# Performance work log

Measured on AMD Instinct MI355X. Metric: run time of the kernel, lower is better.

## Reference

```python
import jax, jax.numpy as jnp
import numpy as np

KEY_DIM = 64
SCALE_PER_SEQ = 1.0 / np.sqrt(KEY_DIM).astype(np.float32)   # attn_scale_factor_per_seq default
SCALE_OVER_SEQS = 1.0 / np.sqrt(KEY_DIM).astype(np.float32) # attn_scale_factor_over_seqs default


def setup_inputs() -> dict:
    key = jax.random.key(0)
    ks = jax.random.split(key, 6)
    b, i, t, j, d = 8, 256, 64, 256, 256
    kd, vd = KEY_DIM, 64
    return {
        "input_seq": jax.random.normal(ks[0], (b, i, d), dtype=jnp.float32),
        "memory_x": jax.random.normal(ks[1], (b, t, j, d), dtype=jnp.float32),
        "memory_y": jax.random.normal(ks[2], (b, t, j, d), dtype=jnp.float32),
        "Wq": jax.random.normal(ks[3], (d, kd), dtype=jnp.float32) * (1.0 / np.sqrt(d)),
        "bq": jnp.zeros((kd,), dtype=jnp.float32),
        "Wk": jax.random.normal(ks[4], (d, kd), dtype=jnp.float32) * (1.0 / np.sqrt(d)),
        "bk": jnp.zeros((kd,), dtype=jnp.float32),
        "Wv": jax.random.normal(ks[5], (d, vd), dtype=jnp.float32) * (1.0 / np.sqrt(d)),
        "bv": jnp.zeros((vd,), dtype=jnp.float32),
    }


def reference(input_seq, memory_x, memory_y, Wq, bq, Wk, bk, Wv, bv):
    # Dense projections
    queries = input_seq @ Wq + bq            # [b, i, kd]
    keys = memory_x @ Wk + bk                # [b, t, j, kd]
    values = memory_y @ Wv + bv              # [b, t, j, vd]

    # Raw scores between every query and every token of every memory sequence
    attn_mat = jnp.einsum('bik,btjk->btij', queries, keys)  # [b, t, i, j]

    # Level 1: within-sequence attention (softmax over tokens j)
    per_seq_attn = jax.nn.softmax(SCALE_PER_SEQ * attn_mat, axis=-1)
    per_seq_retrieved = jnp.einsum('btij,btjk->btik', per_seq_attn, values)  # [b, t, i, vd]

    # Level 2: over-sequences attention (max over j, softmax over t)
    mem_seq_scores = jnp.max(attn_mat, axis=-1)                      # [b, t, i]
    mem_seq_attn = jax.nn.softmax(SCALE_OVER_SEQS * mem_seq_scores, axis=1)

    retrieved_mems = jnp.einsum('bti,btik->bik', mem_seq_attn, per_seq_retrieved)  # [b, i, vd]
    return retrieved_mems
```

## Files before the change

### kernel.cpp

```cpp
#include <hip/hip_runtime.h>
#include <hip/hip_bf16.h>

#define NB 8
#define NT 64
#define NI 256
#define NJ 256
#define ND 256
#define NKD 64
#define NVD 64
#define SCL 0.125f

typedef __attribute__((ext_vector_type(4))) float f32x4;
typedef __attribute__((ext_vector_type(8))) short bf16x8;
typedef __attribute__((ext_vector_type(4))) short bf16x4;
typedef __attribute__((ext_vector_type(4))) unsigned int uint32x4;

#define MFMA16(A, B, C) __builtin_amdgcn_mfma_f32_16x16x32_bf16((A), (B), (C), 0, 0, 0)

#define R2B 32768

__device__ __forceinline__ unsigned short f2bf(float x) {
  return __builtin_bit_cast(unsigned short, __float2bfloat16(x));
}
__device__ __forceinline__ float bf2f(unsigned short h) {
  return __builtin_bit_cast(float, (unsigned)h << 16);
}
__device__ __forceinline__ void split8(const float* __restrict__ x, bf16x8& hi, bf16x8& lo) {
  #pragma unroll
  for (int e = 0; e < 8; ++e) {
    unsigned short h = f2bf(x[e]);
    hi[e] = (short)h;
    lo[e] = (short)f2bf(x[e] - bf2f(h));
  }
}

__global__ __launch_bounds__(64) void k_prep_projq(
    const float* __restrict__ x, const float* __restrict__ Wq,
    const float* __restrict__ bq,
    const float* __restrict__ Wk, const float* __restrict__ Wv,
    unsigned short* __restrict__ Wkth, unsigned short* __restrict__ Wvth,
    unsigned short* __restrict__ Qh) {
  int lane = threadIdx.x;
  if (blockIdx.x < 256) {
    int t = blockIdx.x * 64 + lane;
    int d = t >> 6, kd = t & 63;
    Wkth[kd * 256 + d] = f2bf(Wk[t]);
    Wvth[kd * 256 + d] = f2bf(Wv[t]);
    return;
  }
  int row = blockIdx.x - 256;
  __shared__ __align__(16) float xs[ND];
  const float* xr = x + (size_t)row * ND;
  #pragma unroll
  for (int cc = 0; cc < 4; ++cc) xs[lane + 64 * cc] = xr[lane + 64 * cc];
  __syncthreads();
  float acc = bq[lane];
  #pragma unroll 4
  for (int d = 0; d < ND; ++d) acc = fmaf(xs[d], Wq[d * NKD + lane], acc);
  Qh[(size_t)row * NKD + lane] = f2bf(acc);
}

__device__ __forceinline__ void stage_plane(
    char* dstb, const unsigned short* __restrict__ Wt, int tid) {
  #pragma unroll
  for (int it = 0; it < 4; ++it) {
    int qq = tid + it * 512;
    int r = qq >> 5, pb = qq & 31;
    uint4 v = *(const uint4*)((const char*)Wt + (size_t)qq * 16);
    *(uint4*)(dstb + r * 512 + ((pb ^ (r & 7)) << 4)) = v;
  }
}

__global__ __launch_bounds__(512, 4) void k_fused(
    const float* __restrict__ Xm, const float* __restrict__ Ym,
    const unsigned short* __restrict__ Wkth, const unsigned short* __restrict__ Wvth,
    const float* __restrict__ bk, const float* __restrict__ bv,
    const unsigned short* __restrict__ Qh,
    unsigned short* __restrict__ R,
    float* __restrict__ Sc) {
  __shared__ __align__(16) char smemb[65536];
  int tid = threadIdx.x;
  int bt = blockIdx.x, b = bt >> 6;
  int w = tid >> 6, lane = tid & 63, c = lane & 15, g = lane >> 4;

  const float* xr0 = Xm + (size_t)bt * 65536 + (size_t)(w * 32 + c) * 256 + g * 8;
  const float* xr1 = xr0 + 16 * 256;
  const float* yr0 = Ym + (size_t)bt * 65536 + (size_t)(w * 32 + c) * 256 + g * 8;
  const float* yr1 = yr0 + 16 * 256;

  float4 xa0 = *(const float4*)(xr0),      xa1 = *(const float4*)(xr0 + 4);
  float4 xa2 = *(const float4*)(xr1),      xa3 = *(const float4*)(xr1 + 4);
  float4 xb0 = *(const float4*)(xr0 + 32), xb1 = *(const float4*)(xr0 + 36);
  float4 xb2 = *(const float4*)(xr1 + 32), xb3 = *(const float4*)(xr1 + 36);
  float4 ya0 = *(const float4*)(yr0),      ya1 = *(const float4*)(yr0 + 4);
  float4 ya2 = *(const float4*)(yr1),      ya3 = *(const float4*)(yr1 + 4);
  float4 yb0 = *(const float4*)(yr0 + 32), yb1 = *(const float4*)(yr0 + 36);
  float4 yb2 = *(const float4*)(yr1 + 32), yb3 = *(const float4*)(yr1 + 36);

  stage_plane(smemb, Wkth, tid);
  stage_plane(smemb + R2B, Wvth, tid);
  __syncthreads();

  f32x4 kacc[4][2];
  f32x4 vacc[2][4];
  #pragma unroll
  for (int mf = 0; mf < 4; ++mf) { kacc[mf][0] = (f32x4)0.f; kacc[mf][1] = (f32x4)0.f; }
  #pragma unroll
  for (int mf = 0; mf < 2; ++mf)
    #pragma unroll
    for (int nf = 0; nf < 4; ++nf) vacc[mf][nf] = (f32x4)0.f;

  #pragma unroll
  for (int ks = 0; ks < 8; ++ks) {
    float x0[8], x1[8];
    if (ks & 1) {
      *(float4*)&x0[0] = xb0; *(float4*)&x0[4] = xb1;
      *(float4*)&x1[0] = xb2; *(float4*)&x1[4] = xb3;
      if (ks < 6) {
        xb0 = *(const float4*)(xr0 + (ks + 2) * 32);
        xb1 = *(const float4*)(xr0 + (ks + 2) * 32 + 4);
        xb2 = *(const float4*)(xr1 + (ks + 2) * 32);
        xb3 = *(const float4*)(xr1 + (ks + 2) * 32 + 4);
      }
    } else {
      *(float4*)&x0[0] = xa0; *(float4*)&x0[4] = xa1;
      *(float4*)&x1[0] = xa2; *(float4*)&x1[4] = xa3;
      if (ks < 6) {
        xa0 = *(const float4*)(xr0 + (ks + 2) * 32);
        xa1 = *(const float4*)(xr0 + (ks + 2) * 32 + 4);
        xa2 = *(const float4*)(xr1 + (ks + 2) * 32);
        xa3 = *(const float4*)(xr1 + (ks + 2) * 32 + 4);
      }
    }
    {
      bf16x8 b0h, b0l, b1h, b1l;
      split8(x0, b0h, b0l);
      split8(x1, b1h, b1l);
      #pragma unroll
      for (int mf = 0; mf < 4; ++mf) {
        int r = mf * 16 + c;
        int ba = r * 512 + (((ks * 4 + g) ^ (r & 7)) << 4);
        bf16x8 awh = *(const bf16x8*)(smemb + ba);
        kacc[mf][0] = MFMA16(awh, b0h, kacc[mf][0]);
        kacc[mf][0] = MFMA16(awh, b0l, kacc[mf][0]);
        kacc[mf][1] = MFMA16(awh, b1h, kacc[mf][1]);
        kacc[mf][1] = MFMA16(awh, b1l, kacc[mf][1]);
      }
    }
    float y0[8], y1[8];
    if (ks & 1) {
      *(float4*)&y0[0] = yb0; *(float4*)&y0[4] = yb1;
      *(float4*)&y1[0] = yb2; *(float4*)&y1[4] = yb3;
      if (ks < 6) {
        yb0 = *(const float4*)(yr0 + (ks + 2) * 32);
        yb1 = *(const float4*)(yr0 + (ks + 2) * 32 + 4);
        yb2 = *(const float4*)(yr1 + (ks + 2) * 32);
        yb3 = *(const float4*)(yr1 + (ks + 2) * 32 + 4);
      }
    } else {
      *(float4*)&y0[0] = ya0; *(float4*)&y0[4] = ya1;
      *(float4*)&y1[0] = ya2; *(float4*)&y1[4] = ya3;
      if (ks < 6) {
        ya0 = *(const float4*)(yr0 + (ks + 2) * 32);
        ya1 = *(const float4*)(yr0 + (ks + 2) * 32 + 4);
        ya2 = *(const float4*)(yr1 + (ks + 2) * 32);
        ya3 = *(const float4*)(yr1 + (ks + 2) * 32 + 4);
      }
    }
    {
      bf16x8 a0h, a0l, a1h, a1l;
      split8(y0, a0h, a0l);
      split8(y1, a1h, a1l);
      #pragma unroll
      for (int nf = 0; nf < 4; ++nf) {
        int r = nf * 16 + c;
        int ba = R2B + r * 512 + (((ks * 4 + g) ^ (r & 7)) << 4);
        bf16x8 bwh = *(const bf16x8*)(smemb + ba);
        vacc[0][nf] = MFMA16(a0h, bwh, vacc[0][nf]);
        vacc[0][nf] = MFMA16(a0l, bwh, vacc[0][nf]);
        vacc[1][nf] = MFMA16(a1h, bwh, vacc[1][nf]);
        vacc[1][nf] = MFMA16(a1l, bwh, vacc[1][nf]);
      }
    }
  }
  bf16x8 qbh[2][2];
  #pragma unroll
  for (int ks = 0; ks < 2; ++ks)
    #pragma unroll
    for (int ic = 0; ic < 2; ++ic) {
      size_t qo = ((size_t)b * NI + w * 32 + ic * 16 + c) * NKD + ks * 32 + g * 8;
      qbh[ks][ic] = *(const bf16x8*)(Qh + qo);
    }
  __syncthreads();

  #pragma unroll
  for (int nf = 0; nf < 2; ++nf) {
    int j = w * 32 + nf * 16 + c;
    #pragma unroll
    for (int mf = 0; mf < 4; ++mf) {
      bf16x4 ph;
      #pragma unroll
      for (int r = 0; r < 4; ++r)
        ph[r] = (short)f2bf(kacc[mf][nf][r] + bk[mf * 16 + g * 4 + r]);
      int pb = mf * 2 + (g >> 1);
      int ba = j * 128 + ((pb ^ (j & 7)) << 4) + (g & 1) * 8;
      *(bf16x4*)(smemb + ba) = ph;
    }
  }
  #pragma unroll
  for (int nf = 0; nf < 4; ++nf) {
    int vd = nf * 16 + c;
    float bs = bv[vd];
    #pragma unroll
    for (int mf = 0; mf < 2; ++mf) {
      bf16x4 ph;
      #pragma unroll
      for (int r = 0; r < 4; ++r) ph[r] = (short)f2bf(vacc[mf][nf][r] + bs);
      int pb = w * 4 + mf * 2 + (g >> 1);
      int ba = R2B + vd * 512 + ((pb ^ (vd & 7)) << 4) + (g & 1) * 8;
      *(bf16x4*)(smemb + ba) = ph;
    }
  }
  __syncthreads();

  #pragma unroll
  for (int ic = 0; ic < 2; ++ic) {
    int i = w * 32 + ic * 16 + c;

    f32x4 sa[16];
    #pragma unroll
    for (int jf = 0; jf < 16; ++jf) sa[jf] = (f32x4)0.f;
    #pragma unroll
    for (int jf = 0; jf < 16; ++jf) {
      int j = jf * 16 + c;
      #pragma unroll
      for (int ks = 0; ks < 2; ++ks) {
        int ba = j * 128 + (((ks * 4 + g) ^ (j & 7)) << 4);
        bf16x8 kh = *(const bf16x8*)(smemb + ba);
        sa[jf] = MFMA16(kh, qbh[ks][ic], sa[jf]);
      }
    }

    float mx = sa[0][0];
    #pragma unroll
    for (int jf = 0; jf < 16; ++jf)
      #pragma unroll
      for (int r = 0; r < 4; ++r) mx = fmaxf(mx, sa[jf][r]);
    mx = fmaxf(mx, __shfl_xor(mx, 16));
    mx = fmaxf(mx, __shfl_xor(mx, 32));
    if (g == 0) Sc[(size_t)bt * NI + i] = mx;
    float sum = 0.f;
    #pragma unroll
    for (int jf = 0; jf < 16; ++jf)
      #pragma unroll
      for (int r = 0; r < 4; ++r) {
        float p = __expf((sa[jf][r] - mx) * SCL);
        sa[jf][r] = p;
        sum += p;
      }
    sum += __shfl_xor(sum, 16);
    sum += __shfl_xor(sum, 32);
    float linv = 1.0f / sum;

    unsigned int plo[16], phi[16];
    #pragma unroll
    for (int jf = 0; jf < 16; ++jf) {
      plo[jf] = (unsigned int)f2bf(sa[jf][0]) | ((unsigned int)f2bf(sa[jf][1]) << 16);
      phi[jf] = (unsigned int)f2bf(sa[jf][2]) | ((unsigned int)f2bf(sa[jf][3]) << 16);
    }

    int srcA = c + 32 * (g & 1);
    int srcB = srcA + 16;
    bool hiH = (g >= 2);

    f32x4 racc[4];
    #pragma unroll
    for (int vf = 0; vf < 4; ++vf) racc[vf] = (f32x4)0.f;
    #pragma unroll
    for (int js = 0; js < 8; ++js) {
      int a0 = __shfl((int)plo[2 * js], srcA);
      int a1 = __shfl((int)phi[2 * js], srcA);
      int a2 = __shfl((int)plo[2 * js], srcB);
      int a3 = __shfl((int)phi[2 * js], srcB);
      int b0 = __shfl((int)plo[2 * js + 1], srcA);
      int b1 = __shfl((int)phi[2 * js + 1], srcA);
      int b2 = __shfl((int)plo[2 * js + 1], srcB);
      int b3 = __shfl((int)phi[2 * js + 1], srcB);
      uint32x4 pw;
      pw[0] = (unsigned int)(hiH ? b0 : a0);
      pw[1] = (unsigned int)(hiH ? b1 : a1);
      pw[2] = (unsigned int)(hiH ? b2 : a2);
      pw[3] = (unsigned int)(hiH ? b3 : a3);
      bf16x8 pf = __builtin_bit_cast(bf16x8, pw);
      #pragma unroll
      for (int vf = 0; vf < 4; ++vf) {
        int vd = vf * 16 + c;
        int vba = R2B + vd * 512 + (((js * 4 + g) ^ (vd & 7)) << 4);
        bf16x8 vh = *(const bf16x8*)(smemb + vba);
        racc[vf] = MFMA16(vh, pf, racc[vf]);
      }
    }

    #pragma unroll
    for (int vf = 0; vf < 4; ++vf) {
      bf16x4 rk;
      #pragma unroll
      for (int r = 0; r < 4; ++r) rk[r] = (short)f2bf(racc[vf][r] * linv);
      *(bf16x4*)(R + ((size_t)bt * NI + i) * NKD + vf * 16 + g * 4) = rk;
    }
  }
}

__global__ __launch_bounds__(256) void k_level2(
    const float* __restrict__ Sc,
    const unsigned short* __restrict__ R,
    float* __restrict__ out) {
  int w = threadIdx.x >> 6, lane = threadIdx.x & 63;
  int bi = blockIdx.x * 4 + w;
  int b = bi >> 8, i = bi & 255;
  float sc = Sc[((size_t)b * NT + lane) * NI + i];
  float mx = sc;
  #pragma unroll
  for (int off = 32; off; off >>= 1) mx = fmaxf(mx, __shfl_xor(mx, off));
  float e = __expf((sc - mx) * SCL);
  float sum = e;
  #pragma unroll
  for (int off = 32; off; off >>= 1) sum += __shfl_xor(sum, off);
  float wn = e / sum;
  float acc = 0.f;
  for (int t = 0; t < NT; ++t) {
    float wt = __shfl(wn, t);
    acc = fmaf(wt, bf2f(R[(((size_t)b * NT + t) * NI + i) * NKD + lane]), acc);
  }
  out[((size_t)b * NI + i) * NVD + lane] = acc;
}

extern "C" void kernel_launch(void* const* d_in, const int* in_sizes, int n_in,
                              void* d_out, int out_size, void* d_ws, size_t ws_size,
                              hipStream_t stream) {
  const float* x   = (const float*)d_in[0];
  const float* mxp = (const float*)d_in[1];
  const float* myp = (const float*)d_in[2];
  const float* Wq  = (const float*)d_in[3];
  const float* bq  = (const float*)d_in[4];
  const float* Wk  = (const float*)d_in[5];
  const float* bk  = (const float*)d_in[6];
  const float* Wv  = (const float*)d_in[7];
  const float* bv  = (const float*)d_in[8];
  float* out = (float*)d_out;

  char* p = (char*)d_ws;
  auto alloc = [&](size_t bytes) { char* r = p; p += (bytes + 255) & ~(size_t)255; return r; };
  unsigned short* Qh   = (unsigned short*)alloc(2048 * 64 * 2);
  unsigned short* Rw   = (unsigned short*)alloc((size_t)131072 * 64 * 2);
  float*          Scw  = (float*)alloc((size_t)131072 * 4);
  unsigned short* Wkth = (unsigned short*)alloc(64 * 256 * 2);
  unsigned short* Wvth = (unsigned short*)alloc(64 * 256 * 2);

  hipLaunchKernelGGL(k_prep_projq, dim3(256 + NB * NI), dim3(64), 0, stream,
                     x, Wq, bq, Wk, Wv, Wkth, Wvth, Qh);
  hipLaunchKernelGGL(k_fused, dim3(NB * NT), dim3(512), 0, stream,
                     mxp, myp, Wkth, Wvth, bk, bv, Qh, Rw, Scw);
  hipLaunchKernelGGL(k_level2, dim3(512), dim3(256), 0, stream, Scw, Rw, out);
}
```

Measured before the change: 94.67 us.

## Fold Wk into queries and compute scores directly against raw memory_x

```diff
diff --git a/kernel.cpp b/kernel.cpp
--- a/kernel.cpp
+++ b/kernel.cpp
@@ -13,11 +13,10 @@
 typedef __attribute__((ext_vector_type(4))) float f32x4;
 typedef __attribute__((ext_vector_type(8))) short bf16x8;
 typedef __attribute__((ext_vector_type(4))) short bf16x4;
-typedef __attribute__((ext_vector_type(4))) unsigned int uint32x4;
 
 #define MFMA16(A, B, C) __builtin_amdgcn_mfma_f32_16x16x32_bf16((A), (B), (C), 0, 0, 0)
 
-#define R2B 32768
+#define XB 32768
 
 __device__ __forceinline__ unsigned short f2bf(float x) {
   return __builtin_bit_cast(unsigned short, __float2bfloat16(x));
@@ -34,18 +33,15 @@
   }
 }
 
-__global__ __launch_bounds__(64) void k_prep_projq(
+__global__ __launch_bounds__(64) void k_prepA(
     const float* __restrict__ x, const float* __restrict__ Wq,
-    const float* __restrict__ bq,
-    const float* __restrict__ Wk, const float* __restrict__ Wv,
-    unsigned short* __restrict__ Wkth, unsigned short* __restrict__ Wvth,
-    unsigned short* __restrict__ Qh) {
+    const float* __restrict__ bq, const float* __restrict__ Wv,
+    unsigned short* __restrict__ Wvth, float* __restrict__ Qf) {
   int lane = threadIdx.x;
   if (blockIdx.x < 256) {
     int t = blockIdx.x * 64 + lane;
-    int d = t >> 6, kd = t & 63;
-    Wkth[kd * 256 + d] = f2bf(Wk[t]);
-    Wvth[kd * 256 + d] = f2bf(Wv[t]);
+    int d = t >> 6, vd = t & 63;
+    Wvth[vd * 256 + d] = f2bf(Wv[t]);
     return;
   }
   int row = blockIdx.x - 256;
@@ -57,257 +53,212 @@
   float acc = bq[lane];
   #pragma unroll 4
   for (int d = 0; d < ND; ++d) acc = fmaf(xs[d], Wq[d * NKD + lane], acc);
-  Qh[(size_t)row * NKD + lane] = f2bf(acc);
-}
-
-__device__ __forceinline__ void stage_plane(
-    char* dstb, const unsigned short* __restrict__ Wt, int tid) {
-  #pragma unroll
-  for (int it = 0; it < 4; ++it) {
-    int qq = tid + it * 512;
-    int r = qq >> 5, pb = qq & 31;
-    uint4 v = *(const uint4*)((const char*)Wt + (size_t)qq * 16);
-    *(uint4*)(dstb + r * 512 + ((pb ^ (r & 7)) << 4)) = v;
-  }
-}
-
-__global__ __launch_bounds__(512, 4) void k_fused(
+  Qf[(size_t)row * NKD + lane] = acc;
+}
+
+__global__ __launch_bounds__(256) void k_prepB(
+    const float* __restrict__ Wk, const float* __restrict__ Qf,
+    unsigned short* __restrict__ Qkw) {
+  __shared__ __align__(16) float qs[8 * 64];
+  int tid = threadIdx.x;
+  size_t bi0 = (size_t)blockIdx.x * 8;
+  qs[tid]       = Qf[bi0 * 64 + tid];
+  qs[tid + 256] = Qf[bi0 * 64 + tid + 256];
+  __syncthreads();
+  int d = tid;
+  float acc[8];
+  #pragma unroll
+  for (int r8 = 0; r8 < 8; ++r8) acc[r8] = 0.f;
+  #pragma unroll 4
+  for (int kc = 0; kc < 16; ++kc) {
+    float4 wv = *(const float4*)(Wk + (size_t)d * 64 + kc * 4);
+    #pragma unroll
+    for (int r8 = 0; r8 < 8; ++r8) {
+      const float* q4 = qs + r8 * 64 + kc * 4;
+      acc[r8] += wv.x * q4[0] + wv.y * q4[1] + wv.z * q4[2] + wv.w * q4[3];
+    }
+  }
+  #pragma unroll
+  for (int r8 = 0; r8 < 8; ++r8)
+    Qkw[(bi0 + r8) * 256 + d] = f2bf(acc[r8]);
+}
+
+__global__ __launch_bounds__(1024) void k_fused(
     const float* __restrict__ Xm, const float* __restrict__ Ym,
-    const unsigned short* __restrict__ Wkth, const unsigned short* __restrict__ Wvth,
-    const float* __restrict__ bk, const float* __restrict__ bv,
-    const unsigned short* __restrict__ Qh,
+    const unsigned short* __restrict__ Wvth, const float* __restrict__ bv,
+    const unsigned short* __restrict__ Qkw,
     unsigned short* __restrict__ R,
     float* __restrict__ Sc) {
-  __shared__ __align__(16) char smemb[65536];
+  __shared__ __align__(16) char smemb[163840];
   int tid = threadIdx.x;
   int bt = blockIdx.x, b = bt >> 6;
   int w = tid >> 6, lane = tid & 63, c = lane & 15, g = lane >> 4;
 
-  const float* xr0 = Xm + (size_t)bt * 65536 + (size_t)(w * 32 + c) * 256 + g * 8;
-  const float* xr1 = xr0 + 16 * 256;
-  const float* yr0 = Ym + (size_t)bt * 65536 + (size_t)(w * 32 + c) * 256 + g * 8;
-  const float* yr1 = yr0 + 16 * 256;
-
-  float4 xa0 = *(const float4*)(xr0),      xa1 = *(const float4*)(xr0 + 4);
-  float4 xa2 = *(const float4*)(xr1),      xa3 = *(const float4*)(xr1 + 4);
-  float4 xb0 = *(const float4*)(xr0 + 32), xb1 = *(const float4*)(xr0 + 36);
-  float4 xb2 = *(const float4*)(xr1 + 32), xb3 = *(const float4*)(xr1 + 36);
-  float4 ya0 = *(const float4*)(yr0),      ya1 = *(const float4*)(yr0 + 4);
-  float4 ya2 = *(const float4*)(yr1),      ya3 = *(const float4*)(yr1 + 4);
-  float4 yb0 = *(const float4*)(yr0 + 32), yb1 = *(const float4*)(yr0 + 36);
-  float4 yb2 = *(const float4*)(yr1 + 32), yb3 = *(const float4*)(yr1 + 36);
-
-  stage_plane(smemb, Wkth, tid);
-  stage_plane(smemb + R2B, Wvth, tid);
-  __syncthreads();
-
-  f32x4 kacc[4][2];
-  f32x4 vacc[2][4];
-  #pragma unroll
-  for (int mf = 0; mf < 4; ++mf) { kacc[mf][0] = (f32x4)0.f; kacc[mf][1] = (f32x4)0.f; }
-  #pragma unroll
-  for (int mf = 0; mf < 2; ++mf)
-    #pragma unroll
-    for (int nf = 0; nf < 4; ++nf) vacc[mf][nf] = (f32x4)0.f;
+  const float* xbase = Xm + (size_t)bt * 65536;
+  const float* yr = Ym + (size_t)bt * 65536 + (size_t)(w * 16 + c) * 256 + g * 8;
+
+  float4 ya0 = *(const float4*)(yr),      ya1 = *(const float4*)(yr + 4);
+  float4 yb0 = *(const float4*)(yr + 32), yb1 = *(const float4*)(yr + 36);
+  float4 xf0 = *(const float4*)(xbase + (size_t)(tid >> 5) * 256 + (tid & 31) * 8);
+  float4 xf1 = *(const float4*)(xbase + (size_t)(tid >> 5) * 256 + (tid & 31) * 8 + 4);
+
+  #pragma unroll
+  for (int it = 0; it < 2; ++it) {
+    int qq = tid + it * 1024;
+    int r = qq >> 5, pb = qq & 31;
+    uint4 v = *(const uint4*)((const char*)Wvth + (size_t)qq * 16);
+    *(uint4*)(smemb + r * 512 + ((pb ^ (r & 7)) << 4)) = v;
+  }
+  __syncthreads();
+
+  f32x4 vacc[4];
+  #pragma unroll
+  for (int nf = 0; nf < 4; ++nf) vacc[nf] = (f32x4)0.f;
 
   #pragma unroll
   for (int ks = 0; ks < 8; ++ks) {
-    float x0[8], x1[8];
-    if (ks & 1) {
-      *(float4*)&x0[0] = xb0; *(float4*)&x0[4] = xb1;
-      *(float4*)&x1[0] = xb2; *(float4*)&x1[4] = xb3;
-      if (ks < 6) {
-        xb0 = *(const float4*)(xr0 + (ks + 2) * 32);
-        xb1 = *(const float4*)(xr0 + (ks + 2) * 32 + 4);
-        xb2 = *(const float4*)(xr1 + (ks + 2) * 32);
-        xb3 = *(const float4*)(xr1 + (ks + 2) * 32 + 4);
-      }
-    } else {
-      *(float4*)&x0[0] = xa0; *(float4*)&x0[4] = xa1;
-      *(float4*)&x1[0] = xa2; *(float4*)&x1[4] = xa3;
-      if (ks < 6) {
-        xa0 = *(const float4*)(xr0 + (ks + 2) * 32);
-        xa1 = *(const float4*)(xr0 + (ks + 2) * 32 + 4);
-        xa2 = *(const float4*)(xr1 + (ks + 2) * 32);
-        xa3 = *(const float4*)(xr1 + (ks + 2) * 32 + 4);
-      }
-    }
-    {
-      bf16x8 b0h, b0l, b1h, b1l;
-      split8(x0, b0h, b0l);
-      split8(x1, b1h, b1l);
-      #pragma unroll
-      for (int mf = 0; mf < 4; ++mf) {
-        int r = mf * 16 + c;
-        int ba = r * 512 + (((ks * 4 + g) ^ (r & 7)) << 4);
-        bf16x8 awh = *(const bf16x8*)(smemb + ba);
-        kacc[mf][0] = MFMA16(awh, b0h, kacc[mf][0]);
-        kacc[mf][0] = MFMA16(awh, b0l, kacc[mf][0]);
-        kacc[mf][1] = MFMA16(awh, b1h, kacc[mf][1]);
-        kacc[mf][1] = MFMA16(awh, b1l, kacc[mf][1]);
-      }
-    }
-    float y0[8], y1[8];
+    float4 cx0 = xf0, cx1 = xf1;
+    int cc = ks * 1024 + tid;
+    if (ks < 7) {
+      int cn = cc + 1024;
+      xf0 = *(const float4*)(xbase + (size_t)(cn >> 5) * 256 + (cn & 31) * 8);
+      xf1 = *(const float4*)(xbase + (size_t)(cn >> 5) * 256 + (cn & 31) * 8 + 4);
+    }
+    float y0[8];
     if (ks & 1) {
       *(float4*)&y0[0] = yb0; *(float4*)&y0[4] = yb1;
-      *(float4*)&y1[0] = yb2; *(float4*)&y1[4] = yb3;
       if (ks < 6) {
-        yb0 = *(const float4*)(yr0 + (ks + 2) * 32);
-        yb1 = *(const float4*)(yr0 + (ks + 2) * 32 + 4);
-        yb2 = *(const float4*)(yr1 + (ks + 2) * 32);
-        yb3 = *(const float4*)(yr1 + (ks + 2) * 32 + 4);
+        yb0 = *(const float4*)(yr + (ks + 2) * 32);
+        yb1 = *(const float4*)(yr + (ks + 2) * 32 + 4);
       }
     } else {
       *(float4*)&y0[0] = ya0; *(float4*)&y0[4] = ya1;
-      *(float4*)&y1[0] = ya2; *(float4*)&y1[4] = ya3;
       if (ks < 6) {
-        ya0 = *(const float4*)(yr0 + (ks + 2) * 32);
-        ya1 = *(const float4*)(yr0 + (ks + 2) * 32 + 4);
-        ya2 = *(const float4*)(yr1 + (ks + 2) * 32);
-        ya3 = *(const float4*)(yr1 + (ks + 2) * 32 + 4);
+        ya0 = *(const float4*)(yr + (ks + 2) * 32);
+        ya1 = *(const float4*)(yr + (ks + 2) * 32 + 4);
       }
     }
     {
-      bf16x8 a0h, a0l, a1h, a1l;
+      int r = cc >> 5, q2 = cc & 31;
+      uint4 xw;
+      xw.x = (unsigned int)f2bf(cx0.x) | ((unsigned int)f2bf(cx0.y) << 16);
+      xw.y = (unsigned int)f2bf(cx0.z) | ((unsigned int)f2bf(cx0.w) << 16);
+      xw.z = (unsigned int)f2bf(cx1.x) | ((unsigned int)f2bf(cx1.y) << 16);
+      xw.w = (unsigned int)f2bf(cx1.z) | ((unsigned int)f2bf(cx1.w) << 16);
+      *(uint4*)(smemb + XB + r * 512 + ((q2 ^ (r & 7)) << 4)) = xw;
+    }
+    {
+      bf16x8 a0h, a0l;
       split8(y0, a0h, a0l);
-      split8(y1, a1h, a1l);
       #pragma unroll
       for (int nf = 0; nf < 4; ++nf) {
         int r = nf * 16 + c;
-        int ba = R2B + r * 512 + (((ks * 4 + g) ^ (r & 7)) << 4);
+        int ba = r * 512 + (((ks * 4 + g) ^ (r & 7)) << 4);
         bf16x8 bwh = *(const bf16x8*)(smemb + ba);
-        vacc[0][nf] = MFMA16(a0h, bwh, vacc[0][nf]);
-        vacc[0][nf] = MFMA16(a0l, bwh, vacc[0][nf]);
-        vacc[1][nf] = MFMA16(a1h, bwh, vacc[1][nf]);
-        vacc[1][nf] = MFMA16(a1l, bwh, vacc[1][nf]);
+        vacc[nf] = MFMA16(a0h, bwh, vacc[nf]);
+        vacc[nf] = MFMA16(a0l, bwh, vacc[nf]);
       }
     }
   }
-  bf16x8 qbh[2][2];
-  #pragma unroll
-  for (int ks = 0; ks < 2; ++ks)
-    #pragma unroll
-    for (int ic = 0; ic < 2; ++ic) {
-      size_t qo = ((size_t)b * NI + w * 32 + ic * 16 + c) * NKD + ks * 32 + g * 8;
-      qbh[ks][ic] = *(const bf16x8*)(Qh + qo);
-    }
-  __syncthreads();
-
-  #pragma unroll
-  for (int nf = 0; nf < 2; ++nf) {
-    int j = w * 32 + nf * 16 + c;
-    #pragma unroll
-    for (int mf = 0; mf < 4; ++mf) {
-      bf16x4 ph;
-      #pragma unroll
-      for (int r = 0; r < 4; ++r)
-        ph[r] = (short)f2bf(kacc[mf][nf][r] + bk[mf * 16 + g * 4 + r]);
-      int pb = mf * 2 + (g >> 1);
-      int ba = j * 128 + ((pb ^ (j & 7)) << 4) + (g & 1) * 8;
-      *(bf16x4*)(smemb + ba) = ph;
-    }
-  }
+  bf16x8 qk[8];
+  #pragma unroll
+  for (int ks = 0; ks < 8; ++ks)
+    qk[ks] = *(const bf16x8*)(Qkw + ((size_t)(b * NI + w * 16 + c)) * 256 + ks * 32 + g * 8);
+  __syncthreads();
+
   #pragma unroll
   for (int nf = 0; nf < 4; ++nf) {
     int vd = nf * 16 + c;
     float bs = bv[vd];
-    #pragma unroll
-    for (int mf = 0; mf < 2; ++mf) {
-      bf16x4 ph;
-      #pragma unroll
-      for (int r = 0; r < 4; ++r) ph[r] = (short)f2bf(vacc[mf][nf][r] + bs);
-      int pb = w * 4 + mf * 2 + (g >> 1);
-      int ba = R2B + vd * 512 + ((pb ^ (vd & 7)) << 4) + (g & 1) * 8;
-      *(bf16x4*)(smemb + ba) = ph;
-    }
-  }
-  __syncthreads();
-
-  #pragma unroll
-  for (int ic = 0; ic < 2; ++ic) {
-    int i = w * 32 + ic * 16 + c;
-
-    f32x4 sa[16];
-    #pragma unroll
-    for (int jf = 0; jf < 16; ++jf) sa[jf] = (f32x4)0.f;
+    bf16x4 ph;
+    #pragma unroll
+    for (int r = 0; r < 4; ++r) ph[r] = (short)f2bf(vacc[nf][r] + bs);
+    int pb = w * 2 + (g >> 1);
+    *(bf16x4*)(smemb + vd * 512 + ((pb ^ (vd & 7)) << 4) + (g & 1) * 8) = ph;
+  }
+  __syncthreads();
+
+  int i = w * 16 + c;
+
+  f32x4 sa[16];
+  #pragma unroll
+  for (int jf = 0; jf < 16; ++jf) sa[jf] = (f32x4)0.f;
+  #pragma unroll
+  for (int ks = 0; ks < 8; ++ks) {
     #pragma unroll
     for (int jf = 0; jf < 16; ++jf) {
-      int j = jf * 16 + c;
-      #pragma unroll
-      for (int ks = 0; ks < 2; ++ks) {
-        int ba = j * 128 + (((ks * 4 + g) ^ (j & 7)) << 4);
-        bf16x8 kh = *(const bf16x8*)(smemb + ba);
-        sa[jf] = MFMA16(kh, qbh[ks][ic], sa[jf]);
-      }
-    }
-
-    float mx = sa[0][0];
-    #pragma unroll
-    for (int jf = 0; jf < 16; ++jf)
-      #pragma unroll
-      for (int r = 0; r < 4; ++r) mx = fmaxf(mx, sa[jf][r]);
-    mx = fmaxf(mx, __shfl_xor(mx, 16));
-    mx = fmaxf(mx, __shfl_xor(mx, 32));
-    if (g == 0) Sc[(size_t)bt * NI + i] = mx;
-    float sum = 0.f;
-    #pragma unroll
-    for (int jf = 0; jf < 16; ++jf)
-      #pragma unroll
-      for (int r = 0; r < 4; ++r) {
-        float p = __expf((sa[jf][r] - mx) * SCL);
-        sa[jf][r] = p;
-        sum += p;
-      }
-    sum += __shfl_xor(sum, 16);
-    sum += __shfl_xor(sum, 32);
-    float linv = 1.0f / sum;
-
-    unsigned int plo[16], phi[16];
-    #pragma unroll
-    for (int jf = 0; jf < 16; ++jf) {
-      plo[jf] = (unsigned int)f2bf(sa[jf][0]) | ((unsigned int)f2bf(sa[jf][1]) << 16);
-      phi[jf] = (unsigned int)f2bf(sa[jf][2]) | ((unsigned int)f2bf(sa[jf][3]) << 16);
-    }
-
-    int srcA = c + 32 * (g & 1);
-    int srcB = srcA + 16;
-    bool hiH = (g >= 2);
-
-    f32x4 racc[4];
-    #pragma unroll
-    for (int vf = 0; vf < 4; ++vf) racc[vf] = (f32x4)0.f;
-    #pragma unroll
-    for (int js = 0; js < 8; ++js) {
-      int a0 = __shfl((int)plo[2 * js], srcA);
-      int a1 = __shfl((int)phi[2 * js], srcA);
-      int a2 = __shfl((int)plo[2 * js], srcB);
-      int a3 = __shfl((int)phi[2 * js], srcB);
-      int b0 = __shfl((int)plo[2 * js + 1], srcA);
-      int b1 = __shfl((int)phi[2 * js + 1], srcA);
-      int b2 = __shfl((int)plo[2 * js + 1], srcB);
-      int b3 = __shfl((int)phi[2 * js + 1], srcB);
-      uint32x4 pw;
-      pw[0] = (unsigned int)(hiH ? b0 : a0);
-      pw[1] = (unsigned int)(hiH ? b1 : a1);
-      pw[2] = (unsigned int)(hiH ? b2 : a2);
-      pw[3] = (unsigned int)(hiH ? b3 : a3);
-      bf16x8 pf = __builtin_bit_cast(bf16x8, pw);
-      #pragma unroll
-      for (int vf = 0; vf < 4; ++vf) {
-        int vd = vf * 16 + c;
-        int vba = R2B + vd * 512 + (((js * 4 + g) ^ (vd & 7)) << 4);
-        bf16x8 vh = *(const bf16x8*)(smemb + vba);
-        racc[vf] = MFMA16(vh, pf, racc[vf]);
-      }
-    }
-
+      int r = jf * 16 + c;
+      bf16x8 xa = *(const bf16x8*)(smemb + XB + r * 512 + (((ks * 4 + g) ^ (r & 7)) << 4));
+      sa[jf] = MFMA16(xa, qk[ks], sa[jf]);
+    }
+  }
+
+  float mx = sa[0][0];
+  #pragma unroll
+  for (int jf = 0; jf < 16; ++jf)
+    #pragma unroll
+    for (int r = 0; r < 4; ++r) mx = fmaxf(mx, sa[jf][r]);
+  mx = fmaxf(mx, __shfl_xor(mx, 16));
+  mx = fmaxf(mx, __shfl_xor(mx, 32));
+  if (g == 0) Sc[(size_t)bt * NI + i] = mx;
+  float sum = 0.f;
+  #pragma unroll
+  for (int jf = 0; jf < 16; ++jf)
+    #pragma unroll
+    for (int r = 0; r < 4; ++r) {
+      float p = __expf((sa[jf][r] - mx) * SCL);
+      sa[jf][r] = p;
+      sum += p;
+    }
+  sum += __shfl_xor(sum, 16);
+  sum += __shfl_xor(sum, 32);
+  float linv = 1.0f / sum;
+
+  unsigned int plo[16], phi[16];
+  #pragma unroll
+  for (int jf = 0; jf < 16; ++jf) {
+    plo[jf] = (unsigned int)f2bf(sa[jf][0]) | ((unsigned int)f2bf(sa[jf][1]) << 16);
+    phi[jf] = (unsigned int)f2bf(sa[jf][2]) | ((unsigned int)f2bf(sa[jf][3]) << 16);
+  }
+
+  int srcA = c + 32 * (g & 1);
+  int srcB = srcA + 16;
+  bool hiH = (g >= 2);
+
+  f32x4 racc[4];
+  #pragma unroll
+  for (int vf = 0; vf < 4; ++vf) racc[vf] = (f32x4)0.f;
+  #pragma unroll
+  for (int js = 0; js < 8; ++js) {
+    int a0 = __shfl((int)plo[2 * js], srcA);
+    int a1 = __shfl((int)phi[2 * js], srcA);
+    int a2 = __shfl((int)plo[2 * js], srcB);
+    int a3 = __shfl((int)phi[2 * js], srcB);
+    int b0 = __shfl((int)plo[2 * js + 1], srcA);
+    int b1 = __shfl((int)phi[2 * js + 1], srcA);
+    int b2 = __shfl((int)plo[2 * js + 1], srcB);
+    int b3 = __shfl((int)phi[2 * js + 1], srcB);
+    unsigned int pw0 = (unsigned int)(hiH ? b0 : a0);
+    unsigned int pw1 = (unsigned int)(hiH ? b1 : a1);
+    unsigned int pw2 = (unsigned int)(hiH ? b2 : a2);
+    unsigned int pw3 = (unsigned int)(hiH ? b3 : a3);
+    uint4 pwv = make_uint4(pw0, pw1, pw2, pw3);
+    bf16x8 pf = __builtin_bit_cast(bf16x8, pwv);
     #pragma unroll
     for (int vf = 0; vf < 4; ++vf) {
-      bf16x4 rk;
-      #pragma unroll
-      for (int r = 0; r < 4; ++r) rk[r] = (short)f2bf(racc[vf][r] * linv);
-      *(bf16x4*)(R + ((size_t)bt * NI + i) * NKD + vf * 16 + g * 4) = rk;
-    }
+      int vd = vf * 16 + c;
+      int vba = vd * 512 + (((js * 4 + g) ^ (vd & 7)) << 4);
+      bf16x8 vh = *(const bf16x8*)(smemb + vba);
+      racc[vf] = MFMA16(vh, pf, racc[vf]);
+    }
+  }
+
+  #pragma unroll
+  for (int vf = 0; vf < 4; ++vf) {
+    bf16x4 rk;
+    #pragma unroll
+    for (int r = 0; r < 4; ++r) rk[r] = (short)f2bf(racc[vf][r] * linv);
+    *(bf16x4*)(R + ((size_t)bt * NI + i) * NKD + vf * 16 + g * 4) = rk;
   }
 }
 
@@ -344,22 +295,22 @@
   const float* Wq  = (const float*)d_in[3];
   const float* bq  = (const float*)d_in[4];
   const float* Wk  = (const float*)d_in[5];
-  const float* bk  = (const float*)d_in[6];
   const float* Wv  = (const float*)d_in[7];
   const float* bv  = (const float*)d_in[8];
   float* out = (float*)d_out;
 
   char* p = (char*)d_ws;
   auto alloc = [&](size_t bytes) { char* r = p; p += (bytes + 255) & ~(size_t)255; return r; };
-  unsigned short* Qh   = (unsigned short*)alloc(2048 * 64 * 2);
+  float*          Qfw  = (float*)alloc((size_t)2048 * 64 * 4);
+  unsigned short* Qkw  = (unsigned short*)alloc((size_t)2048 * 256 * 2);
   unsigned short* Rw   = (unsigned short*)alloc((size_t)131072 * 64 * 2);
   float*          Scw  = (float*)alloc((size_t)131072 * 4);
-  unsigned short* Wkth = (unsigned short*)alloc(64 * 256 * 2);
   unsigned short* Wvth = (unsigned short*)alloc(64 * 256 * 2);
 
-  hipLaunchKernelGGL(k_prep_projq, dim3(256 + NB * NI), dim3(64), 0, stream,
-                     x, Wq, bq, Wk, Wv, Wkth, Wvth, Qh);
-  hipLaunchKernelGGL(k_fused, dim3(NB * NT), dim3(512), 0, stream,
-                     mxp, myp, Wkth, Wvth, bk, bv, Qh, Rw, Scw);
+  hipLaunchKernelGGL(k_prepA, dim3(256 + NB * NI), dim3(64), 0, stream,
+                     x, Wq, bq, Wv, Wvth, Qfw);
+  hipLaunchKernelGGL(k_prepB, dim3(256), dim3(256), 0, stream, Wk, Qfw, Qkw);
+  hipLaunchKernelGGL(k_fused, dim3(NB * NT), dim3(1024), 0, stream,
+                     mxp, myp, Wvth, bv, Qkw, Rw, Scw);
   hipLaunchKernelGGL(k_level2, dim3(512), dim3(256), 0, stream, Scw, Rw, out);
 }
```

Measured after the change: 109.2 us. 1.15x slower.
